# Kernel optimization log

Hardware: AMD Instinct MI355X
Metric: run time of the kernel (lower is better)

Reference implementation:

```python
import jax, jax.numpy as jnp
import numpy as np

T = 8192   # sequence length (steps)
H = 1024   # hidden_size


def _unif(key, shape, scale):
    return jax.random.uniform(key, shape, minval=-scale, maxval=scale, dtype=jnp.float32)


def setup_inputs() -> dict:
    key = jax.random.key(0)
    ks = jax.random.split(key, 14)
    s_in = 1.0 / np.sqrt(1.0)   # nn.Linear(1, H) init bound
    s_h = 1.0 / np.sqrt(H)      # LSTM / Linear(H, 1) init bound
    d = {}
    d["inputs"] = jax.random.normal(ks[0], (T, 1), dtype=jnp.float32)
    # input projection: Linear(1, H)
    d["W_in"] = _unif(ks[1], (H, 1), s_in)
    d["b_in"] = _unif(ks[2], (H,), s_in)
    # LSTM layer 0 (gate order i, f, g, o as in PyTorch)
    d["W_ih0"] = _unif(ks[3], (4 * H, H), s_h)
    d["W_hh0"] = _unif(ks[4], (4 * H, H), s_h)
    d["b_ih0"] = _unif(ks[5], (4 * H,), s_h)
    d["b_hh0"] = _unif(ks[6], (4 * H,), s_h)
    # LSTM layer 1
    d["W_ih1"] = _unif(ks[7], (4 * H, H), s_h)
    d["W_hh1"] = _unif(ks[8], (4 * H, H), s_h)
    d["b_ih1"] = _unif(ks[9], (4 * H,), s_h)
    d["b_hh1"] = _unif(ks[10], (4 * H,), s_h)
    # output projection: Linear(H, 1)
    d["W_out"] = _unif(ks[11], (1, H), s_h)
    d["b_out"] = _unif(ks[12], (1,), s_h)
    return d


def _lstm_cell(x, h, c, W_ih, W_hh, b):
    # x, h, c: [H]; W_ih, W_hh: [4H, H]; b: [4H]
    gates = x @ W_ih.T + h @ W_hh.T + b
    i, f, g, o = jnp.split(gates, 4, axis=-1)
    c_new = jax.nn.sigmoid(f) * c + jax.nn.sigmoid(i) * jnp.tanh(g)
    h_new = jax.nn.sigmoid(o) * jnp.tanh(c_new)
    return h_new, c_new


def reference(inputs, W_in, b_in, W_ih0, W_hh0, b_ih0, b_hh0,
              W_ih1, W_hh1, b_ih1, b_hh1, W_out, b_out):
    # Teacher forcing (force=True): per-step input is inputs[i].
    # Vectorize the per-step input projection across all timesteps: [T, H]
    x_all = inputs @ W_in.T + b_in
    b0 = b_ih0 + b_hh0
    b1 = b_ih1 + b_hh1

    def step(carry, x):
        h0, c0, h1, c1 = carry
        h0, c0 = _lstm_cell(x, h0, c0, W_ih0, W_hh0, b0)
        h1, c1 = _lstm_cell(h0, h1, c1, W_ih1, W_hh1, b1)
        return (h0, c0, h1, c1), h1

    z = jnp.zeros((H,), dtype=x_all.dtype)
    (h0, c0, h1, c1), hs = jax.lax.scan(step, (z, z, z, z), x_all)
    # Vectorized output projection: [T, 1] -> [T, 1, 1] to match torch outputs
    outputs = (hs @ W_out.T + b_out)[:, None, :]
    return outputs
```

## Files before the change

kernel.cpp:

```cpp
#include <hip/hip_runtime.h>

#define T_STEPS 8192
#define HDIM 1024
#define NL0 64
#define NL1 128
#define NWG (NL0 + NL1)
#define RING 64
#define RMASK 63
#define PVALVE 400000L
typedef unsigned long long u64;
typedef unsigned int u32x4 __attribute__((ext_vector_type(4)));

__device__ __forceinline__ float wred(float v) {
#pragma unroll
    for (int s = 32; s >= 1; s >>= 1) v += __shfl_xor(v, s, 64);
    return v;
}
__device__ __forceinline__ int wred_min(int v) {
#pragma unroll
    for (int s = 32; s >= 1; s >>= 1) v = min(v, __shfl_xor(v, s, 64));
    return v;
}
__device__ __forceinline__ float sigm(float x) { return 1.0f / (1.0f + expf(-x)); }

__device__ __forceinline__ void st_coh_i32(int* p, int v) {
    asm volatile("global_store_dword %0, %1, off sc0 sc1" :: "v"(p), "v"(v) : "memory");
}
__device__ __forceinline__ int ld_coh_i32(const int* p) {
    int v;
    asm volatile("global_load_dword %0, %1, off sc0 sc1\n\ts_waitcnt vmcnt(0)"
                 : "=&v"(v) : "v"(p) : "memory");
    return v;
}
__device__ __forceinline__ void st_pair(u64* p, u64 v) {
    asm volatile("global_store_dwordx2 %0, %1, off sc0 sc1" :: "v"(p), "v"(v) : "memory");
}
__device__ __forceinline__ u32x4 ld_q16(const void* p) {
    u32x4 v;
    asm volatile("global_load_dwordx4 %0, %1, off sc0 sc1\n\ts_waitcnt vmcnt(0)"
                 : "=&v"(v) : "v"(p) : "memory");
    return v;
}
__device__ __forceinline__ void ld_q32(const void* p, u32x4& a, u32x4& b) {
    asm volatile(
        "global_load_dwordx4 %0, %2, off sc0 sc1\n\t"
        "global_load_dwordx4 %1, %2, off offset:16 sc0 sc1\n\t"
        "s_waitcnt vmcnt(0)"
        : "=&v"(a), "=&v"(b) : "v"(p) : "memory");
}
__device__ __forceinline__ void st_q16(void* p, u32x4 v) {
    asm volatile("global_store_dwordx4 %0, %1, off sc0 sc1" :: "v"(p), "v"(v) : "memory");
}
__device__ __forceinline__ void ld3i(const int* p, int& a, int& b, int& c) {
    asm volatile(
        "global_load_dword %0, %3, off sc0 sc1\n\t"
        "global_load_dword %1, %3, off offset:256 sc0 sc1\n\t"
        "global_load_dword %2, %3, off offset:512 sc0 sc1\n\t"
        "s_waitcnt vmcnt(0)"
        : "=&v"(a), "=&v"(b), "=&v"(c) : "v"(p) : "memory");
}
__device__ __forceinline__ u64 pack(float h, int tag) {
    return ((u64)(unsigned)tag << 32) | (u64)__float_as_uint(h);
}

__global__ void lstm_prologue(const float* __restrict__ Wih0, const float* __restrict__ Win,
                              const float* __restrict__ bin, const float* __restrict__ bih0,
                              const float* __restrict__ bhh0, const float* __restrict__ bih1,
                              const float* __restrict__ bhh1,
                              float* __restrict__ U, float* __restrict__ V, float* __restrict__ B1) {
    const int wv = threadIdx.x >> 6, lane = threadIdx.x & 63;
    const int r = blockIdx.x * 4 + wv;
    const float* wp = Wih0 + (size_t)r * HDIM;
    float au = 0.f, av = 0.f;
#pragma unroll
    for (int j = 0; j < 16; ++j) {
        float wj = wp[lane + 64 * j];
        au += wj * Win[lane + 64 * j];
        av += wj * bin[lane + 64 * j];
    }
    au = wred(au);
    av = wred(av);
    if (lane == 0) {
        U[r] = au;
        V[r] = av + bih0[r] + bhh0[r];
        B1[r] = bih1[r] + bhh1[r];
    }
}

__global__ __launch_bounds__(512, 1) void lstm_persistent(
    const float* __restrict__ inputs, const float* __restrict__ Whh0,
    const float* __restrict__ Wih1, const float* __restrict__ Whh1,
    const float* __restrict__ Wout, int* flags, u64* h0q, u64* h1q,
    const float* __restrict__ U, const float* __restrict__ V, const float* __restrict__ B1,
    float* part) {
    __shared__ float kbuf[2][2048];
    __shared__ float ibuf[T_STEPS];
    __shared__ float osum[2][8];
    __shared__ int lds_ab;
    const int tid = threadIdx.x;
    const int wv = tid >> 6;
    const int lane = tid & 63;
    const int wg = blockIdx.x;
    int* abp = flags + 1024;
    const int* frep = flags + 256 + (wg & 31) * 16;

    if (wg == NWG) {
        if (tid >= 64) return;
        long it = 0;
        for (;;) {
            int a, b, c;
            ld3i(flags + lane, a, b, c);
            int m = wred_min(min(a, min(b, c)));
            if (lane < 32) st_coh_i32(flags + 256 + lane * 16, m);
            if (m >= T_STEPS) break;
            asm volatile("s_sleep 1");
            if ((++it & 63) == 0) {
                if (ld_coh_i32(abp)) break;
                if (it > PVALVE) { if (lane == 0) st_coh_i32(abp, 1); break; }
            }
        }
        return;
    }

    if (tid == 0) lds_ab = 0;

    if (wg < NL0) {
        const int base_e = wg * 16 + wv * 2;
        float w[8][16];
        float uu[2][4], vv[2][4];
#pragma unroll
        for (int j = 0; j < 2; ++j)
#pragma unroll
            for (int g = 0; g < 4; ++g) {
                const int row = g * HDIM + base_e + j;
                const float* pw = Whh0 + (size_t)row * HDIM;
#pragma unroll
                for (int k = 0; k < 16; ++k) w[j * 4 + g][k] = pw[lane + 64 * k];
                uu[j][g] = U[row];
                vv[j][g] = V[row];
            }
#pragma unroll
        for (int k = 0; k < 16; ++k) ibuf[tid + 512 * k] = inputs[tid + 512 * k];
        __syncthreads();

        float c0 = 0.f, c1 = 0.f;
        for (int p = 0; p < T_STEPS; ++p) {
            const int par = p & 1;
            u32x4 q = {0, 0, 0, 0};
            if (p > 0) {
                const char* src = (const char*)(h0q + (size_t)((p - 1) & RMASK) * 1024) + 16 * tid;
                const unsigned xt = (unsigned)p;
                bool need = true, ab = false;
                long it = 0;
                for (;;) {
                    if (!__ballot(need)) break;
                    if (need) {
                        q = ld_q16(src);
                        need = !(q.y == xt && q.w == xt);
                    }
                    if ((++it & 255) == 0) {
                        if (ld_coh_i32(abp) || it > PVALVE) {
                            st_coh_i32(abp, 1); ab = true; break;
                        }
                    }
                }
                if (ab) lds_ab = 1;
            }
            kbuf[par][2 * tid] = __uint_as_float(q.x);
            kbuf[par][2 * tid + 1] = __uint_as_float(q.z);
            __syncthreads();
            if (lds_ab) break;
            if ((p & 3) == 3 && tid == 0) st_coh_i32(flags + wg, p + 1);
            float hv[16];
#pragma unroll
            for (int j = 0; j < 16; ++j) hv[j] = kbuf[par][lane + 64 * j];
            float acc[8];
#pragma unroll
            for (int r = 0; r < 8; ++r) {
                float s = 0.f;
#pragma unroll
                for (int k = 0; k < 16; ++k) s += w[r][k] * hv[k];
                acc[r] = s;
            }
#pragma unroll
            for (int r = 0; r < 8; ++r) acc[r] = wred(acc[r]);
            const float st = ibuf[p];
            float gi = acc[0] + st * uu[0][0] + vv[0][0];
            float gf = acc[1] + st * uu[0][1] + vv[0][1];
            float gg = acc[2] + st * uu[0][2] + vv[0][2];
            float go = acc[3] + st * uu[0][3] + vv[0][3];
            float cn0 = sigm(gf) * c0 + sigm(gi) * tanhf(gg);
            float hn0 = sigm(go) * tanhf(cn0);
            c0 = cn0;
            gi = acc[4] + st * uu[1][0] + vv[1][0];
            gf = acc[5] + st * uu[1][1] + vv[1][1];
            gg = acc[6] + st * uu[1][2] + vv[1][2];
            go = acc[7] + st * uu[1][3] + vv[1][3];
            float cn1 = sigm(gf) * c1 + sigm(gi) * tanhf(gg);
            float hn1 = sigm(go) * tanhf(cn1);
            c1 = cn1;
            if (p >= 48 && (p & 15) == 0) {
                long itf = 0;
                for (;;) {
                    if (ld_coh_i32(frep) >= p - 44) break;
                    asm volatile("s_sleep 2");
                    if (ld_coh_i32(abp)) { lds_ab = 1; break; }
                    if (++itf > PVALVE) { st_coh_i32(abp, 1); lds_ab = 1; break; }
                }
            }
            if (lane == 0) {
                u32x4 o;
                o.x = __float_as_uint(hn0); o.y = (unsigned)(p + 1);
                o.z = __float_as_uint(hn1); o.w = (unsigned)(p + 1);
                st_q16(h0q + (size_t)(p & RMASK) * 1024 + base_e, o);
            }
        }
        if (tid == 0) st_coh_i32(flags + wg, T_STEPS);
    } else {
        const int wgb = wg - NL0;
        const int e = wgb * 8 + wv;
        const int hl = lane & 31;
        const float* wsrc = (lane < 32) ? Wih1 : Whh1;
        float w[4][32];
        float bb[4];
#pragma unroll
        for (int g = 0; g < 4; ++g) {
            const int row = g * HDIM + e;
            const float* pw = wsrc + (size_t)row * HDIM;
#pragma unroll
            for (int k = 0; k < 32; ++k) w[g][k] = pw[hl + 32 * k];
            bb[g] = B1[row];
        }
        const float woute = Wout[e];
        const int g4 = (wv & 3) * 64 + lane;
        __syncthreads();

        float c1s = 0.f;
        for (int t = 0; t < T_STEPS; ++t) {
            const int par = t & 1;
            u32x4 qa = {0, 0, 0, 0}, qb = {0, 0, 0, 0};
            const bool skip = (wv >= 4) && (t == 0);
            if (!skip) {
                const char* src = (wv < 4)
                    ? (const char*)(h0q + (size_t)(t & RMASK) * 1024) + 32 * g4
                    : (const char*)(h1q + (size_t)((t - 1) & RMASK) * 1024) + 32 * g4;
                const unsigned xt = (wv < 4) ? (unsigned)(t + 1) : (unsigned)t;
                bool need = true, ab = false;
                long it = 0;
                for (;;) {
                    if (!__ballot(need)) break;
                    if (need) {
                        ld_q32(src, qa, qb);
                        need = !((qa.y == xt) & (qa.w == xt) & (qb.y == xt) & (qb.w == xt));
                    }
                    if ((++it & 255) == 0) {
                        if (ld_coh_i32(abp) || it > PVALVE) {
                            st_coh_i32(abp, 1); ab = true; break;
                        }
                    }
                }
                if (ab) lds_ab = 1;
            }
            {
                const int kb = (wv < 4) ? 4 * g4 : 1024 + 4 * g4;
                kbuf[par][kb] = __uint_as_float(qa.x);
                kbuf[par][kb + 1] = __uint_as_float(qa.z);
                kbuf[par][kb + 2] = __uint_as_float(qb.x);
                kbuf[par][kb + 3] = __uint_as_float(qb.z);
            }
            __syncthreads();
            if (lds_ab) break;
            if (tid == 0) {
                if (t >= 1) {
                    const int q = (t - 1) & 1;
                    float s = osum[q][0] + osum[q][1] + osum[q][2] + osum[q][3] +
                              osum[q][4] + osum[q][5] + osum[q][6] + osum[q][7];
                    part[(size_t)(t - 1) * 128 + wgb] = s;
                }
                if ((t & 3) == 3) st_coh_i32(flags + wg, t + 1);
            }
            const int koff = (lane < 32) ? 0 : 1024;
            float hv[32];
#pragma unroll
            for (int j = 0; j < 32; ++j) hv[j] = kbuf[par][koff + hl + 32 * j];
            float acc[4];
#pragma unroll
            for (int gg2 = 0; gg2 < 4; ++gg2) {
                float s = 0.f;
#pragma unroll
                for (int k = 0; k < 32; ++k) s += w[gg2][k] * hv[k];
                acc[gg2] = s;
            }
#pragma unroll
            for (int gg2 = 0; gg2 < 4; ++gg2) acc[gg2] = wred(acc[gg2]);
            const float gi = acc[0] + bb[0];
            const float gf = acc[1] + bb[1];
            const float gg = acc[2] + bb[2];
            const float go = acc[3] + bb[3];
            const float cn = sigm(gf) * c1s + sigm(gi) * tanhf(gg);
            const float hn = sigm(go) * tanhf(cn);
            c1s = cn;
            if (t >= 48 && (t & 15) == 0) {
                long itf = 0;
                for (;;) {
                    if (ld_coh_i32(frep) >= t - 44) break;
                    asm volatile("s_sleep 2");
                    if (ld_coh_i32(abp)) { lds_ab = 1; break; }
                    if (++itf > PVALVE) { st_coh_i32(abp, 1); lds_ab = 1; break; }
                }
            }
            if (lane == 0) {
                st_pair(h1q + (size_t)(t & RMASK) * 1024 + e, pack(hn, t + 1));
                osum[t & 1][wv] = woute * hn;
            }
        }
        __syncthreads();
        if (tid == 0) {
            const int q = (T_STEPS - 1) & 1;
            float s = osum[q][0] + osum[q][1] + osum[q][2] + osum[q][3] +
                      osum[q][4] + osum[q][5] + osum[q][6] + osum[q][7];
            part[(size_t)(T_STEPS - 1) * 128 + wgb] = s;
            st_coh_i32(flags + wg, T_STEPS);
        }
    }
}

__global__ void lstm_finalize(const float* __restrict__ part, const float* __restrict__ bout,
                              float* __restrict__ out) {
    const int t = blockIdx.x * 256 + threadIdx.x;
    if (t < T_STEPS) {
        const float4* p4 = (const float4*)(part + (size_t)t * 128);
        float s = bout[0];
#pragma unroll
        for (int i = 0; i < 32; ++i) {
            float4 v = p4[i];
            s += v.x + v.y + v.z + v.w;
        }
        out[t] = s;
    }
}

extern "C" void kernel_launch(void* const* d_in, const int* in_sizes, int n_in,
                              void* d_out, int out_size, void* d_ws, size_t ws_size,
                              hipStream_t stream) {
    const float* inputs = (const float*)d_in[0];
    const float* Win  = (const float*)d_in[1];
    const float* bin  = (const float*)d_in[2];
    const float* Wih0 = (const float*)d_in[3];
    const float* Whh0 = (const float*)d_in[4];
    const float* bih0 = (const float*)d_in[5];
    const float* bhh0 = (const float*)d_in[6];
    const float* Wih1 = (const float*)d_in[7];
    const float* Whh1 = (const float*)d_in[8];
    const float* bih1 = (const float*)d_in[9];
    const float* bhh1 = (const float*)d_in[10];
    const float* Wout = (const float*)d_in[11];
    const float* bout = (const float*)d_in[12];

    char* ws = (char*)d_ws;
    int*  flags = (int*)ws;
    u64*  h0q   = (u64*)(ws + 8192);
    u64*  h1q   = (u64*)(ws + 8192 + 524288);
    float* U    = (float*)(ws + 1056768);
    float* V    = (float*)(ws + 1073152);
    float* B1   = (float*)(ws + 1089536);
    float* part = (float*)(ws + 1105920);

    if (ws_size < (size_t)5300224) return;

    hipMemsetAsync(ws, 0, 8192, stream);

    lstm_prologue<<<1024, 256, 0, stream>>>(Wih0, Win, bin, bih0, bhh0, bih1, bhh1, U, V, B1);
    lstm_persistent<<<NWG + 1, 512, 0, stream>>>(inputs, Whh0, Wih1, Whh1, Wout,
                                                 flags, h0q, h1q, U, V, B1, part);
    lstm_finalize<<<(T_STEPS + 255) / 256, 256, 0, stream>>>(part, bout, (float*)d_out);
}
```

Baseline: 40.20 ms.

## Double workgroup size to 1024 threads, one hidden unit per wave in both layers

Workgroups of the persistent LSTM kernel grow from 512 to 1024 threads. Each layer-0 wave now computes one hidden unit instead of two, and each layer-1 unit is split across two waves (input and recurrent halves) whose partial sums are combined through shared memory. Each thread polls one 8-byte tagged entry per step instead of wider 16/32-byte loads. The aim is to halve the per-wave dot-product work on the serial critical path. The cost is an extra barrier and a single-wave gate finalization in layer 1, plus more polling threads contending on coherent memory. The flow-control window changes from every 16 steps with lag 44 to every 8 steps with lag 40.

```diff
diff --git a/kernel.cpp b/kernel.cpp
--- a/kernel.cpp
+++ b/kernel.cpp
@@ -5,11 +5,9 @@
 #define NL0 64
 #define NL1 128
 #define NWG (NL0 + NL1)
-#define RING 64
 #define RMASK 63
 #define PVALVE 400000L
 typedef unsigned long long u64;
-typedef unsigned int u32x4 __attribute__((ext_vector_type(4)));
 
 __device__ __forceinline__ float wred(float v) {
 #pragma unroll
@@ -35,21 +33,11 @@
 __device__ __forceinline__ void st_pair(u64* p, u64 v) {
     asm volatile("global_store_dwordx2 %0, %1, off sc0 sc1" :: "v"(p), "v"(v) : "memory");
 }
-__device__ __forceinline__ u32x4 ld_q16(const void* p) {
-    u32x4 v;
-    asm volatile("global_load_dwordx4 %0, %1, off sc0 sc1\n\ts_waitcnt vmcnt(0)"
+__device__ __forceinline__ u64 ld_p8(const u64* p) {
+    u64 v;
+    asm volatile("global_load_dwordx2 %0, %1, off sc0 sc1\n\ts_waitcnt vmcnt(0)"
                  : "=&v"(v) : "v"(p) : "memory");
     return v;
-}
-__device__ __forceinline__ void ld_q32(const void* p, u32x4& a, u32x4& b) {
-    asm volatile(
-        "global_load_dwordx4 %0, %2, off sc0 sc1\n\t"
-        "global_load_dwordx4 %1, %2, off offset:16 sc0 sc1\n\t"
-        "s_waitcnt vmcnt(0)"
-        : "=&v"(a), "=&v"(b) : "v"(p) : "memory");
-}
-__device__ __forceinline__ void st_q16(void* p, u32x4 v) {
-    asm volatile("global_store_dwordx4 %0, %1, off sc0 sc1" :: "v"(p), "v"(v) : "memory");
 }
 __device__ __forceinline__ void ld3i(const int* p, int& a, int& b, int& c) {
     asm volatile(
@@ -62,6 +50,8 @@
 __device__ __forceinline__ u64 pack(float h, int tag) {
     return ((u64)(unsigned)tag << 32) | (u64)__float_as_uint(h);
 }
+__device__ __forceinline__ float pval(u64 q) { return __uint_as_float((unsigned)q); }
+__device__ __forceinline__ unsigned ptag(u64 q) { return (unsigned)(q >> 32); }
 
 __global__ void lstm_prologue(const float* __restrict__ Wih0, const float* __restrict__ Win,
                               const float* __restrict__ bin, const float* __restrict__ bih0,
@@ -87,15 +77,18 @@
     }
 }
 
-__global__ __launch_bounds__(512, 1) void lstm_persistent(
+__global__ __launch_bounds__(1024, 1) void lstm_persistent(
     const float* __restrict__ inputs, const float* __restrict__ Whh0,
     const float* __restrict__ Wih1, const float* __restrict__ Whh1,
     const float* __restrict__ Wout, int* flags, u64* h0q, u64* h1q,
     const float* __restrict__ U, const float* __restrict__ V, const float* __restrict__ B1,
     float* part) {
-    __shared__ float kbuf[2][2048];
+    __shared__ float kb0[2][1024];
+    __shared__ float kb1[2][1024];
     __shared__ float ibuf[T_STEPS];
-    __shared__ float osum[2][8];
+    __shared__ float psum[16][4];
+    __shared__ float bld[32], wolds[8];
+    __shared__ float osum[2];
     __shared__ int lds_ab;
     const int tid = threadIdx.x;
     const int wv = tid >> 6;
@@ -125,202 +118,177 @@
     if (tid == 0) lds_ab = 0;
 
     if (wg < NL0) {
-        const int base_e = wg * 16 + wv * 2;
-        float w[8][16];
-        float uu[2][4], vv[2][4];
-#pragma unroll
-        for (int j = 0; j < 2; ++j)
-#pragma unroll
-            for (int g = 0; g < 4; ++g) {
-                const int row = g * HDIM + base_e + j;
-                const float* pw = Whh0 + (size_t)row * HDIM;
-#pragma unroll
-                for (int k = 0; k < 16; ++k) w[j * 4 + g][k] = pw[lane + 64 * k];
-                uu[j][g] = U[row];
-                vv[j][g] = V[row];
-            }
-#pragma unroll
-        for (int k = 0; k < 16; ++k) ibuf[tid + 512 * k] = inputs[tid + 512 * k];
+        const int e0 = wg * 16 + wv;
+        float w0[4][16], uu[4], vv[4];
+#pragma unroll
+        for (int g = 0; g < 4; ++g) {
+            const int row = g * HDIM + e0;
+            const float* pw = Whh0 + (size_t)row * HDIM;
+#pragma unroll
+            for (int k = 0; k < 16; ++k) w0[g][k] = pw[lane + 64 * k];
+            uu[g] = U[row];
+            vv[g] = V[row];
+        }
+#pragma unroll
+        for (int k = 0; k < 8; ++k) ibuf[tid + 1024 * k] = inputs[tid + 1024 * k];
         __syncthreads();
 
-        float c0 = 0.f, c1 = 0.f;
+        float c0 = 0.f;
         for (int p = 0; p < T_STEPS; ++p) {
             const int par = p & 1;
-            u32x4 q = {0, 0, 0, 0};
+            u64 q = 0;
             if (p > 0) {
-                const char* src = (const char*)(h0q + (size_t)((p - 1) & RMASK) * 1024) + 16 * tid;
+                const u64* src = h0q + (size_t)((p - 1) & RMASK) * 1024 + tid;
                 const unsigned xt = (unsigned)p;
-                bool need = true, ab = false;
+                bool need = true;
                 long it = 0;
                 for (;;) {
                     if (!__ballot(need)) break;
-                    if (need) {
-                        q = ld_q16(src);
-                        need = !(q.y == xt && q.w == xt);
-                    }
+                    if (need) { q = ld_p8(src); need = (ptag(q) != xt); }
                     if ((++it & 255) == 0) {
                         if (ld_coh_i32(abp) || it > PVALVE) {
-                            st_coh_i32(abp, 1); ab = true; break;
+                            st_coh_i32(abp, 1); lds_ab = 1; break;
                         }
                     }
                 }
-                if (ab) lds_ab = 1;
-            }
-            kbuf[par][2 * tid] = __uint_as_float(q.x);
-            kbuf[par][2 * tid + 1] = __uint_as_float(q.z);
+            }
+            kb0[par][tid] = pval(q);
             __syncthreads();
             if (lds_ab) break;
             if ((p & 3) == 3 && tid == 0) st_coh_i32(flags + wg, p + 1);
             float hv[16];
 #pragma unroll
-            for (int j = 0; j < 16; ++j) hv[j] = kbuf[par][lane + 64 * j];
-            float acc[8];
-#pragma unroll
-            for (int r = 0; r < 8; ++r) {
+            for (int j = 0; j < 16; ++j) hv[j] = kb0[par][lane + 64 * j];
+            float acc[4];
+#pragma unroll
+            for (int g = 0; g < 4; ++g) {
                 float s = 0.f;
 #pragma unroll
-                for (int k = 0; k < 16; ++k) s += w[r][k] * hv[k];
-                acc[r] = s;
-            }
-#pragma unroll
-            for (int r = 0; r < 8; ++r) acc[r] = wred(acc[r]);
+                for (int k = 0; k < 16; ++k) s += w0[g][k] * hv[k];
+                acc[g] = s;
+            }
+#pragma unroll
+            for (int g = 0; g < 4; ++g) acc[g] = wred(acc[g]);
             const float st = ibuf[p];
-            float gi = acc[0] + st * uu[0][0] + vv[0][0];
-            float gf = acc[1] + st * uu[0][1] + vv[0][1];
-            float gg = acc[2] + st * uu[0][2] + vv[0][2];
-            float go = acc[3] + st * uu[0][3] + vv[0][3];
-            float cn0 = sigm(gf) * c0 + sigm(gi) * tanhf(gg);
-            float hn0 = sigm(go) * tanhf(cn0);
-            c0 = cn0;
-            gi = acc[4] + st * uu[1][0] + vv[1][0];
-            gf = acc[5] + st * uu[1][1] + vv[1][1];
-            gg = acc[6] + st * uu[1][2] + vv[1][2];
-            go = acc[7] + st * uu[1][3] + vv[1][3];
-            float cn1 = sigm(gf) * c1 + sigm(gi) * tanhf(gg);
-            float hn1 = sigm(go) * tanhf(cn1);
-            c1 = cn1;
-            if (p >= 48 && (p & 15) == 0) {
+            const float gi = acc[0] + st * uu[0] + vv[0];
+            const float gf = acc[1] + st * uu[1] + vv[1];
+            const float gg = acc[2] + st * uu[2] + vv[2];
+            const float go = acc[3] + st * uu[3] + vv[3];
+            const float cn = sigm(gf) * c0 + sigm(gi) * tanhf(gg);
+            const float hn = sigm(go) * tanhf(cn);
+            c0 = cn;
+            if (p >= 48 && (p & 7) == 0 && lane == 0) {
                 long itf = 0;
                 for (;;) {
-                    if (ld_coh_i32(frep) >= p - 44) break;
+                    if (ld_coh_i32(frep) >= p - 40) break;
                     asm volatile("s_sleep 2");
-                    if (ld_coh_i32(abp)) { lds_ab = 1; break; }
-                    if (++itf > PVALVE) { st_coh_i32(abp, 1); lds_ab = 1; break; }
-                }
-            }
-            if (lane == 0) {
-                u32x4 o;
-                o.x = __float_as_uint(hn0); o.y = (unsigned)(p + 1);
-                o.z = __float_as_uint(hn1); o.w = (unsigned)(p + 1);
-                st_q16(h0q + (size_t)(p & RMASK) * 1024 + base_e, o);
-            }
-        }
+                    if (ld_coh_i32(abp)) break;
+                    if (++itf > PVALVE) { st_coh_i32(abp, 1); break; }
+                }
+            }
+            if (lane == 0)
+                st_pair(h0q + (size_t)(p & RMASK) * 1024 + e0, pack(hn, p + 1));
+        }
+        __syncthreads();
         if (tid == 0) st_coh_i32(flags + wg, T_STEPS);
     } else {
         const int wgb = wg - NL0;
-        const int e = wgb * 8 + wv;
-        const int hl = lane & 31;
-        const float* wsrc = (lane < 32) ? Wih1 : Whh1;
-        float w[4][32];
-        float bb[4];
+        const int half = wv >> 3;
+        const int ew = wv & 7;
+        const int e = wgb * 8 + ew;
+        const float* wsrc = half ? Whh1 : Wih1;
+        float w1[4][16];
 #pragma unroll
         for (int g = 0; g < 4; ++g) {
             const int row = g * HDIM + e;
             const float* pw = wsrc + (size_t)row * HDIM;
 #pragma unroll
-            for (int k = 0; k < 32; ++k) w[g][k] = pw[hl + 32 * k];
-            bb[g] = B1[row];
-        }
-        const float woute = Wout[e];
-        const int g4 = (wv & 3) * 64 + lane;
+            for (int k = 0; k < 16; ++k) w1[g][k] = pw[lane + 64 * k];
+        }
+        if (tid < 32) bld[tid] = B1[(tid & 3) * HDIM + wgb * 8 + (tid >> 2)];
+        if (tid < 8) wolds[tid] = Wout[wgb * 8 + tid];
         __syncthreads();
 
-        float c1s = 0.f;
+        float cst = 0.f;
         for (int t = 0; t < T_STEPS; ++t) {
             const int par = t & 1;
-            u32x4 qa = {0, 0, 0, 0}, qb = {0, 0, 0, 0};
-            const bool skip = (wv >= 4) && (t == 0);
-            if (!skip) {
-                const char* src = (wv < 4)
-                    ? (const char*)(h0q + (size_t)(t & RMASK) * 1024) + 32 * g4
-                    : (const char*)(h1q + (size_t)((t - 1) & RMASK) * 1024) + 32 * g4;
-                const unsigned xt = (wv < 4) ? (unsigned)(t + 1) : (unsigned)t;
-                bool need = true, ab = false;
+            u64 q0 = 0, q1 = 0;
+            {
+                const u64* s0 = h0q + (size_t)(t & RMASK) * 1024 + tid;
+                const u64* s1 = h1q + (size_t)((t - 1) & RMASK) * 1024 + tid;
+                const unsigned xt0 = (unsigned)(t + 1), xt1 = (unsigned)t;
+                bool n0 = true, n1 = (t > 0);
                 long it = 0;
                 for (;;) {
-                    if (!__ballot(need)) break;
-                    if (need) {
-                        ld_q32(src, qa, qb);
-                        need = !((qa.y == xt) & (qa.w == xt) & (qb.y == xt) & (qb.w == xt));
-                    }
+                    if (!__ballot(n0 | n1)) break;
+                    if (n0) { q0 = ld_p8(s0); n0 = (ptag(q0) != xt0); }
+                    if (n1) { q1 = ld_p8(s1); n1 = (ptag(q1) != xt1); }
                     if ((++it & 255) == 0) {
                         if (ld_coh_i32(abp) || it > PVALVE) {
-                            st_coh_i32(abp, 1); ab = true; break;
+                            st_coh_i32(abp, 1); lds_ab = 1; break;
                         }
                     }
                 }
-                if (ab) lds_ab = 1;
-            }
-            {
-                const int kb = (wv < 4) ? 4 * g4 : 1024 + 4 * g4;
-                kbuf[par][kb] = __uint_as_float(qa.x);
-                kbuf[par][kb + 1] = __uint_as_float(qa.z);
-                kbuf[par][kb + 2] = __uint_as_float(qb.x);
-                kbuf[par][kb + 3] = __uint_as_float(qb.z);
-            }
+            }
+            kb0[par][tid] = pval(q0);
+            kb1[par][tid] = pval(q1);
             __syncthreads();
             if (lds_ab) break;
             if (tid == 0) {
-                if (t >= 1) {
-                    const int q = (t - 1) & 1;
-                    float s = osum[q][0] + osum[q][1] + osum[q][2] + osum[q][3] +
-                              osum[q][4] + osum[q][5] + osum[q][6] + osum[q][7];
-                    part[(size_t)(t - 1) * 128 + wgb] = s;
-                }
-                if ((t & 3) == 3) st_coh_i32(flags + wg, t + 1);
-            }
-            const int koff = (lane < 32) ? 0 : 1024;
-            float hv[32];
-#pragma unroll
-            for (int j = 0; j < 32; ++j) hv[j] = kbuf[par][koff + hl + 32 * j];
+                if (t >= 1) part[(size_t)(t - 1) * 128 + wgb] = osum[(t - 1) & 1];
+                if ((t & 3) == 3) st_coh_i32(flags + NL0 + wgb, t + 1);
+            }
+            float hv[16];
+            const float* kb = half ? kb1[par] : kb0[par];
+#pragma unroll
+            for (int j = 0; j < 16; ++j) hv[j] = kb[lane + 64 * j];
             float acc[4];
 #pragma unroll
-            for (int gg2 = 0; gg2 < 4; ++gg2) {
+            for (int g = 0; g < 4; ++g) {
                 float s = 0.f;
 #pragma unroll
-                for (int k = 0; k < 32; ++k) s += w[gg2][k] * hv[k];
-                acc[gg2] = s;
-            }
-#pragma unroll
-            for (int gg2 = 0; gg2 < 4; ++gg2) acc[gg2] = wred(acc[gg2]);
-            const float gi = acc[0] + bb[0];
-            const float gf = acc[1] + bb[1];
-            const float gg = acc[2] + bb[2];
-            const float go = acc[3] + bb[3];
-            const float cn = sigm(gf) * c1s + sigm(gi) * tanhf(gg);
-            const float hn = sigm(go) * tanhf(cn);
-            c1s = cn;
-            if (t >= 48 && (t & 15) == 0) {
+                for (int k = 0; k < 16; ++k) s += w1[g][k] * hv[k];
+                acc[g] = s;
+            }
+#pragma unroll
+            for (int g = 0; g < 4; ++g) acc[g] = wred(acc[g]);
+            if (lane == 0) {
+                psum[wv][0] = acc[0]; psum[wv][1] = acc[1];
+                psum[wv][2] = acc[2]; psum[wv][3] = acc[3];
+            }
+            __syncthreads();
+            if (t >= 48 && (t & 7) == 0 && tid == 0) {
                 long itf = 0;
                 for (;;) {
-                    if (ld_coh_i32(frep) >= t - 44) break;
+                    if (ld_coh_i32(frep) >= t - 40) break;
                     asm volatile("s_sleep 2");
-                    if (ld_coh_i32(abp)) { lds_ab = 1; break; }
-                    if (++itf > PVALVE) { st_coh_i32(abp, 1); lds_ab = 1; break; }
-                }
-            }
-            if (lane == 0) {
-                st_pair(h1q + (size_t)(t & RMASK) * 1024 + e, pack(hn, t + 1));
-                osum[t & 1][wv] = woute * hn;
+                    if (ld_coh_i32(abp)) break;
+                    if (++itf > PVALVE) { st_coh_i32(abp, 1); break; }
+                }
+            }
+            if (wv == 0) {
+                float wos = 0.f;
+                if (lane < 8) {
+                    const float gi = psum[lane][0] + psum[lane + 8][0] + bld[lane * 4 + 0];
+                    const float gf = psum[lane][1] + psum[lane + 8][1] + bld[lane * 4 + 1];
+                    const float gg = psum[lane][2] + psum[lane + 8][2] + bld[lane * 4 + 2];
+                    const float go = psum[lane][3] + psum[lane + 8][3] + bld[lane * 4 + 3];
+                    const float cn = sigm(gf) * cst + sigm(gi) * tanhf(gg);
+                    const float hn = sigm(go) * tanhf(cn);
+                    cst = cn;
+                    st_pair(h1q + (size_t)(t & RMASK) * 1024 + wgb * 8 + lane, pack(hn, t + 1));
+                    wos = wolds[lane] * hn;
+                }
+                wos += __shfl_xor(wos, 1, 64);
+                wos += __shfl_xor(wos, 2, 64);
+                wos += __shfl_xor(wos, 4, 64);
+                if (lane == 0) osum[t & 1] = wos;
             }
         }
         __syncthreads();
         if (tid == 0) {
-            const int q = (T_STEPS - 1) & 1;
-            float s = osum[q][0] + osum[q][1] + osum[q][2] + osum[q][3] +
-                      osum[q][4] + osum[q][5] + osum[q][6] + osum[q][7];
-            part[(size_t)(T_STEPS - 1) * 128 + wgb] = s;
-            st_coh_i32(flags + wg, T_STEPS);
+            part[(size_t)(T_STEPS - 1) * 128 + wgb] = osum[(T_STEPS - 1) & 1];
+            st_coh_i32(flags + NL0 + wgb, T_STEPS);
         }
     }
 }
@@ -371,7 +339,7 @@
     hipMemsetAsync(ws, 0, 8192, stream);
 
     lstm_prologue<<<1024, 256, 0, stream>>>(Wih0, Win, bin, bih0, bhh0, bih1, bhh1, U, V, B1);
-    lstm_persistent<<<NWG + 1, 512, 0, stream>>>(inputs, Whh0, Wih1, Whh1, Wout,
-                                                 flags, h0q, h1q, U, V, B1, part);
+    lstm_persistent<<<NWG + 1, 1024, 0, stream>>>(inputs, Whh0, Wih1, Whh1, Wout,
+                                                  flags, h0q, h1q, U, V, B1, part);
     lstm_finalize<<<(T_STEPS + 255) / 256, 256, 0, stream>>>(part, bout, (float*)d_out);
 }
```

Result: faster. 37.29 ms (-7.2%).
